# Performance work log

Measured on AMD Instinct MI355X. Metric: run time of the kernel, lower is better.

The kernel has to match this reference:

```python
import jax, jax.numpy as jnp
import numpy as np
from jax import lax


def _lstm_last(x, w_ih, w_hh, b_ih, b_hh):
    # x: [N, T, F]; PyTorch single-layer LSTM, gate order i,f,g,o. Returns last h: [N, H].
    N, T, F = x.shape
    H = w_hh.shape[1]
    x_proj = jnp.einsum('ntf,gf->tng', x, w_ih) + (b_ih + b_hh)  # [T, N, 4H]

    def step(carry, xp):
        h, c = carry
        gates = xp + h @ w_hh.T
        i, f, g, o = jnp.split(gates, 4, axis=-1)
        c = jax.nn.sigmoid(f) * c + jax.nn.sigmoid(i) * jnp.tanh(g)
        h = jax.nn.sigmoid(o) * jnp.tanh(c)
        return (h, c), None

    h0 = jnp.zeros((N, H), x.dtype)
    (h, _), _ = lax.scan(step, (h0, h0), x_proj)
    return h


def _gcn_conv(x, w, b, src, dst, n_nodes):
    # PyG GCNConv: h = D^{-1/2} (A+I) D^{-1/2} (x @ w) + b
    h = x @ w  # [N, out]
    loops = jnp.arange(n_nodes, dtype=src.dtype)
    s = jnp.concatenate([src, loops])
    d = jnp.concatenate([dst, loops])
    deg = jax.ops.segment_sum(jnp.ones_like(d, dtype=h.dtype), d, num_segments=n_nodes)
    dinv = jnp.where(deg > 0, lax.rsqrt(deg), 0.0)
    norm = dinv[s] * dinv[d]  # [E+N]
    msgs = h[s] * norm[:, None]
    out = jax.ops.segment_sum(msgs, d, num_segments=n_nodes)
    return out + b


def setup_inputs() -> dict:
    key = jax.random.key(0)
    ks = jax.random.split(key, 8)
    N, T, F, H, E, C = 50000, 32, 64, 256, 1600000, 2
    s = 0.05
    return {
        'x': jax.random.normal(ks[0], (N, T, F), jnp.float32),
        'edge_index': jax.random.randint(ks[1], (2, E), 0, N, jnp.int64),
        'w_ih': jax.random.normal(ks[2], (4 * H, F), jnp.float32) * s,
        'w_hh': jax.random.normal(ks[3], (4 * H, H), jnp.float32) * s,
        'b_ih': jnp.zeros((4 * H,), jnp.float32),
        'b_hh': jnp.zeros((4 * H,), jnp.float32),
        'w1': jax.random.normal(ks[4], (H, H), jnp.float32) * s,
        'b1': jnp.zeros((H,), jnp.float32),
        'w2': jax.random.normal(ks[5], (H, H // 2), jnp.float32) * s,
        'b2': jnp.zeros((H // 2,), jnp.float32),
        'wc': jax.random.normal(ks[6], (H // 2, C), jnp.float32) * s,
        'bc': jnp.zeros((C,), jnp.float32),
    }


def reference(x, edge_index, w_ih, w_hh, b_ih, b_hh, w1, b1, w2, b2, wc, bc):
    n_nodes = x.shape[0]
    src, dst = edge_index[0], edge_index[1]
    feats = _lstm_last(x, w_ih, w_hh, b_ih, b_hh)          # [N, H]
    feats = jax.nn.relu(_gcn_conv(feats, w1, b1, src, dst, n_nodes))
    feats = jax.nn.relu(_gcn_conv(feats, w2, b2, src, dst, n_nodes))
    logits = feats @ wc + bc
    return jax.nn.softmax(logits, axis=1)
```

## Files before the change

### kernel.cpp

```cpp
#include <hip/hip_runtime.h>
#include <cstdint>
#include <cstddef>

typedef __attribute__((ext_vector_type(8))) short s16x8;
typedef __attribute__((ext_vector_type(4))) float f32x4;
typedef __attribute__((ext_vector_type(4))) unsigned int u32x4;

#define DEV static __device__ __forceinline__

DEV unsigned short f2bf(float f){
  unsigned u = __builtin_bit_cast(unsigned, f);
  unsigned r = u + 0x7FFFu + ((u >> 16) & 1u);
  return (unsigned short)(r >> 16);
}
DEV float bf2f(unsigned short s){
  unsigned u = ((unsigned)s) << 16;
  return __builtin_bit_cast(float, u);
}
DEV float sigf(float v){ return 1.0f / (1.0f + __expf(-v)); }
DEV float tanh_f(float v){ return 1.0f - 2.0f / (__expf(2.0f*v) + 1.0f); }

#define NT 32
#define NF 64
#define NHID 256
#define MR 112
#define RT 7

__global__ void pack_lstm_kernel(const float* __restrict__ w_ih,
                                 const float* __restrict__ w_hh,
                                 unsigned short* __restrict__ wp){
  int idx = blockIdx.x*256 + threadIdx.x;
  if (idx >= 64*10*64) return;
  int lane = idx & 63;
  int kc = (idx >> 6) % 10;
  int ct = idx / 640;
  int col = ct*16 + (lane & 15);
  int kb = kc*32 + (lane >> 4)*8;
#pragma unroll
  for (int j = 0; j < 8; ++j){
    int k = kb + j;
    float v = (k < 256) ? w_hh[(size_t)col*256 + k] : w_ih[(size_t)col*64 + (k-256)];
    wp[(size_t)idx*8 + j] = f2bf(v);
  }
}

__global__ void pack_gemm_kernel(const float* __restrict__ wsrc,
                                 unsigned short* __restrict__ bp,
                                 int nout, int nct){
  int idx = blockIdx.x*256 + threadIdx.x;
  if (idx >= nct*8*64) return;
  int lane = idx & 63;
  int kc = (idx >> 6) & 7;
  int ct = idx >> 9;
  int col = ct*16 + (lane & 15);
  int kb = kc*32 + (lane >> 4)*8;
#pragma unroll
  for (int j = 0; j < 8; ++j)
    bp[(size_t)idx*8 + j] = f2bf(wsrc[(size_t)(kb + j)*nout + col]);
}

__global__ void bias_kernel(const float* __restrict__ bi, const float* __restrict__ bh,
                            float* __restrict__ bias){
  int i = blockIdx.x*256 + threadIdx.x;
  if (i < 1024) bias[i] = bi[i] + bh[i];
}

__global__ void init_nodes_kernel(int* cnt, int* fill, int nn){
  int i = blockIdx.x*256 + threadIdx.x;
  if (i < nn){ cnt[i] = 0; fill[i] = 0; }
}
__global__ void count_kernel(const int* __restrict__ dst, int* cnt, int ne){
  int e = blockIdx.x*256 + threadIdx.x;
  if (e < ne) atomicAdd(&cnt[dst[e]], 1);
}
__global__ void dinv_kernel(const int* __restrict__ cnt, float* dinv, int nn){
  int i = blockIdx.x*256 + threadIdx.x;
  if (i < nn) dinv[i] = rsqrtf((float)(cnt[i] + 1));
}
__global__ void scan_kernel(const int* __restrict__ cnt, int* __restrict__ rp, int nn){
  __shared__ int sums[1024];
  int tid = threadIdx.x;
  int chunk = (nn + 1023) >> 10;
  int beg = tid * chunk, end = beg + chunk; if (end > nn) end = nn; if (beg > nn) beg = nn;
  int s = 0;
  for (int i = beg; i < end; ++i) s += cnt[i];
  sums[tid] = s; __syncthreads();
  for (int off = 1; off < 1024; off <<= 1){
    int add = (tid >= off) ? sums[tid - off] : 0;
    __syncthreads();
    sums[tid] += add;
    __syncthreads();
  }
  int run = (tid > 0) ? sums[tid - 1] : 0;
  for (int i = beg; i < end; ++i){ rp[i] = run; run += cnt[i]; }
  if (tid == 0) rp[nn] = sums[1023];
}
__global__ void fill_kernel(const int* __restrict__ src, const int* __restrict__ dst,
                            const int* __restrict__ rp, int* fill, int* ci, int ne){
  int e = blockIdx.x*256 + threadIdx.x;
  if (e < ne){
    int d = dst[e];
    int p = atomicAdd(&fill[d], 1);
    ci[rp[d] + p] = src[e];
  }
}

DEV void load_x16p(const float* p, unsigned* xs32){
#pragma unroll
  for (int i = 0; i < 4; ++i){
    f32x4 v = ((const f32x4*)p)[i];
    xs32[i*2]   = (unsigned)f2bf(v[0]) | ((unsigned)f2bf(v[1]) << 16);
    xs32[i*2+1] = (unsigned)f2bf(v[2]) | ((unsigned)f2bf(v[3]) << 16);
  }
}

__global__ __launch_bounds__(512, 2)
void lstm_kernel(const float* __restrict__ x, const s16x8* __restrict__ wp,
                 const float* __restrict__ bias, unsigned short* __restrict__ feats0,
                 int nn){
  extern __shared__ char smem[];
  unsigned short (*h_lds)[MR][264] = (unsigned short (*)[MR][264])smem;
  unsigned short (*x_lds)[72] = (unsigned short (*)[72])(smem + (size_t)2*MR*264*2);

  const int tid = threadIdx.x;
  const int w = tid >> 6;
  const int l = tid & 63;
  const int lrow = l & 15;
  const int lhi = l >> 4;
  const int base = blockIdx.x * MR;

  float bv[2][4];
#pragma unroll
  for (int p = 0; p < 2; ++p)
#pragma unroll
    for (int g = 0; g < 4; ++g)
      bv[p][g] = bias[g*256 + (p*8 + w)*16 + lrow];

  float c[2][RT][4];
#pragma unroll
  for (int p = 0; p < 2; ++p)
#pragma unroll
    for (int r = 0; r < RT; ++r)
#pragma unroll
      for (int q = 0; q < 4; ++q) c[p][r][q] = 0.0f;

  {
    unsigned* hz = (unsigned*)smem;
    for (int i = tid; i < MR*264/2; i += 512) hz[i] = 0u;
  }

  const bool xact = (tid < 448);
  const int xr = tid >> 2, xc = tid & 3;
  long xnode = base + xr; if (xnode >= nn) xnode = nn - 1;
  const float* xb = x + (size_t)xnode * NT * NF + xc * 16;

  unsigned xs32[8];
  if (xact){
    load_x16p(xb, xs32);
    u32x4 a = {xs32[0], xs32[1], xs32[2], xs32[3]};
    u32x4 b = {xs32[4], xs32[5], xs32[6], xs32[7]};
    *(u32x4*)&x_lds[xr][xc*16]     = a;
    *(u32x4*)&x_lds[xr][xc*16 + 8] = b;
  }
  __syncthreads();

  for (int t = 0; t < NT; ++t){
    const int tb = t & 1;
    if (xact && (t + 1 < NT)) load_x16p(xb + (size_t)(t+1)*NF, xs32);

#pragma unroll
    for (int p = 0; p < 2; ++p){
      const int ut = p*8 + w;
      f32x4 acc[RT][4];
#pragma unroll
      for (int r = 0; r < RT; ++r)
#pragma unroll
        for (int g = 0; g < 4; ++g)
          acc[r][g] = (f32x4){bv[p][g], bv[p][g], bv[p][g], bv[p][g]};

#pragma unroll
      for (int kc = 0; kc < 10; ++kc){
        s16x8 bfr[4];
#pragma unroll
        for (int g = 0; g < 4; ++g){
          int ct = g*16 + ut;
          bfr[g] = wp[(size_t)(ct*10 + kc)*64 + l];
        }
#pragma unroll
        for (int r = 0; r < RT; ++r){
          s16x8 afr;
          if (kc < 8)
            afr = *(const s16x8*)&h_lds[tb][r*16 + lrow][kc*32 + lhi*8];
          else
            afr = *(const s16x8*)&x_lds[r*16 + lrow][(kc-8)*32 + lhi*8];
#pragma unroll
          for (int g = 0; g < 4; ++g)
            acc[r][g] = __builtin_amdgcn_mfma_f32_16x16x32_bf16(afr, bfr[g], acc[r][g], 0, 0, 0);
        }
      }
#pragma unroll
      for (int r = 0; r < RT; ++r){
#pragma unroll
        for (int q = 0; q < 4; ++q){
          float iv = acc[r][0][q];
          float fv = acc[r][1][q];
          float gv = acc[r][2][q];
          float ov = acc[r][3][q];
          float cv = c[p][r][q];
          cv = sigf(fv)*cv + sigf(iv)*tanh_f(gv);
          c[p][r][q] = cv;
          float hv = sigf(ov)*tanh_f(cv);
          h_lds[tb^1][r*16 + lhi*4 + q][ut*16 + lrow] = f2bf(hv);
        }
      }
    }
    __syncthreads();
    if (xact && (t + 1 < NT)){
      u32x4 a = {xs32[0], xs32[1], xs32[2], xs32[3]};
      u32x4 b = {xs32[4], xs32[5], xs32[6], xs32[7]};
      *(u32x4*)&x_lds[xr][xc*16]     = a;
      *(u32x4*)&x_lds[xr][xc*16 + 8] = b;
    }
    __syncthreads();
  }

#pragma unroll
  for (int i = 0; i < 7; ++i){
    int ch = i*512 + tid;
    int row = ch >> 5, cc = ch & 31;
    long node = base + row;
    if (node < nn){
      s16x8 v = *(const s16x8*)&h_lds[0][row][cc*8];
      *(s16x8*)&feats0[(size_t)node*256 + cc*8] = v;
    }
  }
}

template<int CTPW, int NOUT>
__global__ __launch_bounds__(256)
void gemm_kernel(const unsigned short* __restrict__ A, const s16x8* __restrict__ Bp,
                 unsigned short* __restrict__ Cout, int nn){
  __shared__ __align__(16) unsigned short a_lds[64][264];
  const int tid = threadIdx.x, w = tid >> 6, l = tid & 63, lrow = l & 15, lhi = l >> 4;
  const long m0 = (long)blockIdx.x * 64;
#pragma unroll
  for (int i = 0; i < 8; ++i){
    int ch = i*256 + tid;
    int row = ch >> 5, cc = ch & 31;
    long node = m0 + row; if (node >= nn) node = nn - 1;
    s16x8 v = *(const s16x8*)&A[(size_t)node*256 + cc*8];
    *(s16x8*)&a_lds[row][cc*8] = v;
  }
  __syncthreads();
  f32x4 acc[4][CTPW];
#pragma unroll
  for (int r = 0; r < 4; ++r)
#pragma unroll
    for (int j = 0; j < CTPW; ++j) acc[r][j] = (f32x4){0.f,0.f,0.f,0.f};
#pragma unroll
  for (int kc = 0; kc < 8; ++kc){
    s16x8 bfr[CTPW];
#pragma unroll
    for (int j = 0; j < CTPW; ++j)
      bfr[j] = Bp[(size_t)((w*CTPW + j)*8 + kc)*64 + l];
#pragma unroll
    for (int r = 0; r < 4; ++r){
      s16x8 afr = *(const s16x8*)&a_lds[r*16 + lrow][kc*32 + lhi*8];
#pragma unroll
      for (int j = 0; j < CTPW; ++j)
        acc[r][j] = __builtin_amdgcn_mfma_f32_16x16x32_bf16(afr, bfr[j], acc[r][j], 0, 0, 0);
    }
  }
#pragma unroll
  for (int r = 0; r < 4; ++r)
#pragma unroll
    for (int j = 0; j < CTPW; ++j){
      int col = (w*CTPW + j)*16 + lrow;
#pragma unroll
      for (int q = 0; q < 4; ++q){
        long node = m0 + r*16 + lhi*4 + q;
        if (node < nn) Cout[(size_t)node*NOUT + col] = f2bf(acc[r][j][q]);
      }
    }
}

template<int D>
__global__ __launch_bounds__(256)
void gather_kernel(const unsigned short* __restrict__ tmp, const int* __restrict__ rp,
                   const int* __restrict__ ci, const float* __restrict__ dinv,
                   const float* __restrict__ bvec, unsigned short* __restrict__ outf,
                   int nn){
  const int l = threadIdx.x & 63;
  const int d = blockIdx.x*4 + (threadIdx.x >> 6);
  if (d >= nn) return;
  constexpr int C = D / 64;
  float dv = dinv[d];
  float acc[C];
  if constexpr (D == 256){
    uint2 u = *((const uint2*)(tmp + (size_t)d*256) + l);
    float w0 = dv*dv;
    acc[0] = w0*bf2f((unsigned short)(u.x & 0xffff));
    acc[1] = w0*bf2f((unsigned short)(u.x >> 16));
    acc[2] = w0*bf2f((unsigned short)(u.y & 0xffff));
    acc[3] = w0*bf2f((unsigned short)(u.y >> 16));
  } else {
    unsigned u = *((const unsigned*)(tmp + (size_t)d*128) + l);
    float w0 = dv*dv;
    acc[0] = w0*bf2f((unsigned short)(u & 0xffff));
    acc[1] = w0*bf2f((unsigned short)(u >> 16));
  }
  int e0 = rp[d], e1 = rp[d+1];
  for (int e = e0; e < e1; ++e){
    int s = ci[e];
    float wgt = dv * dinv[s];
    if constexpr (D == 256){
      uint2 u = *((const uint2*)(tmp + (size_t)s*256) + l);
      acc[0] += wgt*bf2f((unsigned short)(u.x & 0xffff));
      acc[1] += wgt*bf2f((unsigned short)(u.x >> 16));
      acc[2] += wgt*bf2f((unsigned short)(u.y & 0xffff));
      acc[3] += wgt*bf2f((unsigned short)(u.y >> 16));
    } else {
      unsigned u = *((const unsigned*)(tmp + (size_t)s*128) + l);
      acc[0] += wgt*bf2f((unsigned short)(u & 0xffff));
      acc[1] += wgt*bf2f((unsigned short)(u >> 16));
    }
  }
  if constexpr (D == 256){
    float o0 = fmaxf(acc[0] + bvec[l*4+0], 0.f);
    float o1 = fmaxf(acc[1] + bvec[l*4+1], 0.f);
    float o2 = fmaxf(acc[2] + bvec[l*4+2], 0.f);
    float o3 = fmaxf(acc[3] + bvec[l*4+3], 0.f);
    uint2 o;
    o.x = (unsigned)f2bf(o0) | ((unsigned)f2bf(o1) << 16);
    o.y = (unsigned)f2bf(o2) | ((unsigned)f2bf(o3) << 16);
    *((uint2*)(outf + (size_t)d*256) + l) = o;
  } else {
    float o0 = fmaxf(acc[0] + bvec[l*2+0], 0.f);
    float o1 = fmaxf(acc[1] + bvec[l*2+1], 0.f);
    *((unsigned*)(outf + (size_t)d*128) + l) = (unsigned)f2bf(o0) | ((unsigned)f2bf(o1) << 16);
  }
}

__global__ __launch_bounds__(256)
void head_kernel(const unsigned short* __restrict__ feats2, const float* __restrict__ wc,
                 const float* __restrict__ bc, float* __restrict__ out, int nn){
  int n = blockIdx.x*256 + threadIdx.x;
  if (n >= nn) return;
  const uint2* row = (const uint2*)(feats2 + (size_t)n*128);
  float d0 = bc[0], d1 = bc[1];
#pragma unroll
  for (int b = 0; b < 32; ++b){
    uint2 u = row[b];
    float f0 = bf2f((unsigned short)(u.x & 0xffff));
    float f1 = bf2f((unsigned short)(u.x >> 16));
    float f2 = bf2f((unsigned short)(u.y & 0xffff));
    float f3 = bf2f((unsigned short)(u.y >> 16));
    int k = b*4;
    d0 += f0*wc[k*2+0] + f1*wc[(k+1)*2+0] + f2*wc[(k+2)*2+0] + f3*wc[(k+3)*2+0];
    d1 += f0*wc[k*2+1] + f1*wc[(k+1)*2+1] + f2*wc[(k+2)*2+1] + f3*wc[(k+3)*2+1];
  }
  float m = fmaxf(d0, d1);
  float e0 = __expf(d0 - m), e1 = __expf(d1 - m);
  float inv = 1.0f / (e0 + e1);
  ((float2*)out)[n] = make_float2(e0*inv, e1*inv);
}

extern "C" void kernel_launch(void* const* d_in, const int* in_sizes, int n_in,
                              void* d_out, int out_size, void* d_ws, size_t ws_size,
                              hipStream_t stream){
  const float* x     = (const float*)d_in[0];
  const int*   ei    = (const int*)d_in[1];
  const float* w_ih  = (const float*)d_in[2];
  const float* w_hh  = (const float*)d_in[3];
  const float* b_ih  = (const float*)d_in[4];
  const float* b_hh  = (const float*)d_in[5];
  const float* w1    = (const float*)d_in[6];
  const float* b1    = (const float*)d_in[7];
  const float* w2    = (const float*)d_in[8];
  const float* b2    = (const float*)d_in[9];
  const float* wc    = (const float*)d_in[10];
  const float* bc    = (const float*)d_in[11];
  float* out = (float*)d_out;

  const int nn = in_sizes[0] / (NT*NF);
  const int ne = in_sizes[1] / 2;
  const int* src = ei;
  const int* dst = ei + ne;

  char* wsp = (char*)d_ws;
  size_t off = 0;
  auto alloc = [&](size_t bytes) -> void* {
    void* p = wsp + off;
    off += (bytes + 255) & ~(size_t)255;
    return p;
  };
  unsigned short* wp     = (unsigned short*)alloc((size_t)64*10*64*8*2);
  float* bias            = (float*)alloc(1024*4);
  unsigned short* w1p    = (unsigned short*)alloc((size_t)16*8*64*8*2);
  unsigned short* w2p    = (unsigned short*)alloc((size_t)8*8*64*8*2);
  int* cnt               = (int*)alloc((size_t)nn*4);
  float* dinv            = (float*)alloc((size_t)nn*4);
  int* rp                = (int*)alloc(((size_t)nn+1)*4);
  int* fillc             = (int*)alloc((size_t)nn*4);
  int* ci                = (int*)alloc((size_t)ne*4);
  unsigned short* slotA  = (unsigned short*)alloc((size_t)nn*256*2);
  unsigned short* slotB  = (unsigned short*)alloc((size_t)nn*256*2);
  unsigned short* feats0 = slotA;
  unsigned short* tmp1   = slotB;
  unsigned short* feats1 = slotA;
  unsigned short* tmp2   = slotB;
  unsigned short* feats2 = slotB + (size_t)nn*128;
  (void)ws_size; (void)n_in; (void)out_size;

  const int nb = (nn + 255)/256;
  const int eb = (ne + 255)/256;

  hipLaunchKernelGGL(pack_lstm_kernel, dim3(160), dim3(256), 0, stream, w_ih, w_hh, wp);
  hipLaunchKernelGGL(pack_gemm_kernel, dim3(32), dim3(256), 0, stream, w1, w1p, 256, 16);
  hipLaunchKernelGGL(pack_gemm_kernel, dim3(16), dim3(256), 0, stream, w2, w2p, 128, 8);
  hipLaunchKernelGGL(bias_kernel, dim3(4), dim3(256), 0, stream, b_ih, b_hh, bias);
  hipLaunchKernelGGL(init_nodes_kernel, dim3(nb), dim3(256), 0, stream, cnt, fillc, nn);
  hipLaunchKernelGGL(count_kernel, dim3(eb), dim3(256), 0, stream, dst, cnt, ne);
  hipLaunchKernelGGL(dinv_kernel, dim3(nb), dim3(256), 0, stream, cnt, dinv, nn);
  hipLaunchKernelGGL(scan_kernel, dim3(1), dim3(1024), 0, stream, cnt, rp, nn);
  hipLaunchKernelGGL(fill_kernel, dim3(eb), dim3(256), 0, stream, src, dst, rp, fillc, ci, ne);

  const int lwg = (nn + MR - 1)/MR;
  const size_t lstm_lds = (size_t)2*MR*264*2 + (size_t)MR*72*2;
  hipLaunchKernelGGL(lstm_kernel, dim3(lwg), dim3(512), lstm_lds, stream,
                     x, (const s16x8*)wp, bias, feats0, nn);

  const int gwg = (nn + 63)/64;
  const int awg = (nn + 3)/4;
  hipLaunchKernelGGL((gemm_kernel<4,256>), dim3(gwg), dim3(256), 0, stream,
                     feats0, (const s16x8*)w1p, tmp1, nn);
  hipLaunchKernelGGL((gather_kernel<256>), dim3(awg), dim3(256), 0, stream,
                     tmp1, rp, ci, dinv, b1, feats1, nn);
  hipLaunchKernelGGL((gemm_kernel<2,128>), dim3(gwg), dim3(256), 0, stream,
                     feats1, (const s16x8*)w2p, tmp2, nn);
  hipLaunchKernelGGL((gather_kernel<128>), dim3(awg), dim3(256), 0, stream,
                     tmp2, rp, ci, dinv, b2, feats2, nn);
  hipLaunchKernelGGL(head_kernel, dim3(nb), dim3(256), 0, stream, feats2, wc, bc, out, nn);
}
```

Before: 3.934 ms.

## Restructure LSTM kernel to 1024 threads, 64 rows, double-buffered x

```diff
diff --git a/kernel.cpp b/kernel.cpp
--- a/kernel.cpp
+++ b/kernel.cpp
@@ -4,7 +4,6 @@
 
 typedef __attribute__((ext_vector_type(8))) short s16x8;
 typedef __attribute__((ext_vector_type(4))) float f32x4;
-typedef __attribute__((ext_vector_type(4))) unsigned int u32x4;
 
 #define DEV static __device__ __forceinline__
 
@@ -23,8 +22,8 @@
 #define NT 32
 #define NF 64
 #define NHID 256
-#define MR 112
-#define RT 7
+#define MR 64
+#define RT 4
 
 __global__ void pack_lstm_kernel(const float* __restrict__ w_ih,
                                  const float* __restrict__ w_hh,
@@ -105,22 +104,13 @@
   }
 }
 
-DEV void load_x16p(const float* p, unsigned* xs32){
-#pragma unroll
-  for (int i = 0; i < 4; ++i){
-    f32x4 v = ((const f32x4*)p)[i];
-    xs32[i*2]   = (unsigned)f2bf(v[0]) | ((unsigned)f2bf(v[1]) << 16);
-    xs32[i*2+1] = (unsigned)f2bf(v[2]) | ((unsigned)f2bf(v[3]) << 16);
-  }
-}
-
-__global__ __launch_bounds__(512, 2)
+__global__ __launch_bounds__(1024, 4)
 void lstm_kernel(const float* __restrict__ x, const s16x8* __restrict__ wp,
                  const float* __restrict__ bias, unsigned short* __restrict__ feats0,
                  int nn){
   extern __shared__ char smem[];
   unsigned short (*h_lds)[MR][264] = (unsigned short (*)[MR][264])smem;
-  unsigned short (*x_lds)[72] = (unsigned short (*)[72])(smem + (size_t)2*MR*264*2);
+  unsigned short (*x_lds)[MR][72] = (unsigned short (*)[MR][72])(smem + (size_t)2*MR*264*2);
 
   const int tid = threadIdx.x;
   const int w = tid >> 6;
@@ -129,104 +119,93 @@
   const int lhi = l >> 4;
   const int base = blockIdx.x * MR;
 
-  float bv[2][4];
-#pragma unroll
-  for (int p = 0; p < 2; ++p)
-#pragma unroll
-    for (int g = 0; g < 4; ++g)
-      bv[p][g] = bias[g*256 + (p*8 + w)*16 + lrow];
-
-  float c[2][RT][4];
-#pragma unroll
-  for (int p = 0; p < 2; ++p)
-#pragma unroll
-    for (int r = 0; r < RT; ++r)
-#pragma unroll
-      for (int q = 0; q < 4; ++q) c[p][r][q] = 0.0f;
+  float bv[4];
+#pragma unroll
+  for (int g = 0; g < 4; ++g)
+    bv[g] = bias[g*256 + w*16 + lrow];
+
+  float c[RT][4];
+#pragma unroll
+  for (int r = 0; r < RT; ++r)
+#pragma unroll
+    for (int q = 0; q < 4; ++q) c[r][q] = 0.0f;
 
   {
     unsigned* hz = (unsigned*)smem;
-    for (int i = tid; i < MR*264/2; i += 512) hz[i] = 0u;
-  }
-
-  const bool xact = (tid < 448);
-  const int xr = tid >> 2, xc = tid & 3;
+    for (int i = tid; i < MR*264/2; i += 1024) hz[i] = 0u;
+  }
+
+  const int xr = tid >> 4, xc = tid & 15;
   long xnode = base + xr; if (xnode >= nn) xnode = nn - 1;
-  const float* xb = x + (size_t)xnode * NT * NF + xc * 16;
-
-  unsigned xs32[8];
-  if (xact){
-    load_x16p(xb, xs32);
-    u32x4 a = {xs32[0], xs32[1], xs32[2], xs32[3]};
-    u32x4 b = {xs32[4], xs32[5], xs32[6], xs32[7]};
-    *(u32x4*)&x_lds[xr][xc*16]     = a;
-    *(u32x4*)&x_lds[xr][xc*16 + 8] = b;
+  const float* xb_ptr = x + (size_t)xnode * NT * NF + xc * 4;
+
+  {
+    f32x4 v = *(const f32x4*)xb_ptr;
+    uint2 s;
+    s.x = (unsigned)f2bf(v[0]) | ((unsigned)f2bf(v[1]) << 16);
+    s.y = (unsigned)f2bf(v[2]) | ((unsigned)f2bf(v[3]) << 16);
+    *(uint2*)&x_lds[0][xr][xc*4] = s;
   }
   __syncthreads();
 
+  int tb = 0, xbuf = 0;
   for (int t = 0; t < NT; ++t){
-    const int tb = t & 1;
-    if (xact && (t + 1 < NT)) load_x16p(xb + (size_t)(t+1)*NF, xs32);
-
-#pragma unroll
-    for (int p = 0; p < 2; ++p){
-      const int ut = p*8 + w;
-      f32x4 acc[RT][4];
-#pragma unroll
-      for (int r = 0; r < RT; ++r)
+    uint2 xs;
+    const bool pf = (t + 1 < NT);
+    if (pf){
+      f32x4 v = *(const f32x4*)(xb_ptr + (size_t)(t+1)*NF);
+      xs.x = (unsigned)f2bf(v[0]) | ((unsigned)f2bf(v[1]) << 16);
+      xs.y = (unsigned)f2bf(v[2]) | ((unsigned)f2bf(v[3]) << 16);
+    }
+
+    f32x4 acc[RT][4];
+#pragma unroll
+    for (int r = 0; r < RT; ++r)
+#pragma unroll
+      for (int g = 0; g < 4; ++g)
+        acc[r][g] = (f32x4){bv[g], bv[g], bv[g], bv[g]};
+
+#pragma unroll
+    for (int kc = 0; kc < 10; ++kc){
+      s16x8 bfr[4];
+#pragma unroll
+      for (int g = 0; g < 4; ++g)
+        bfr[g] = wp[(size_t)((g*16 + w)*10 + kc)*64 + l];
+#pragma unroll
+      for (int r = 0; r < RT; ++r){
+        s16x8 afr;
+        if (kc < 8)
+          afr = *(const s16x8*)&h_lds[tb][r*16 + lrow][kc*32 + lhi*8];
+        else
+          afr = *(const s16x8*)&x_lds[xbuf][r*16 + lrow][(kc-8)*32 + lhi*8];
 #pragma unroll
         for (int g = 0; g < 4; ++g)
-          acc[r][g] = (f32x4){bv[p][g], bv[p][g], bv[p][g], bv[p][g]};
-
-#pragma unroll
-      for (int kc = 0; kc < 10; ++kc){
-        s16x8 bfr[4];
-#pragma unroll
-        for (int g = 0; g < 4; ++g){
-          int ct = g*16 + ut;
-          bfr[g] = wp[(size_t)(ct*10 + kc)*64 + l];
-        }
-#pragma unroll
-        for (int r = 0; r < RT; ++r){
-          s16x8 afr;
-          if (kc < 8)
-            afr = *(const s16x8*)&h_lds[tb][r*16 + lrow][kc*32 + lhi*8];
-          else
-            afr = *(const s16x8*)&x_lds[r*16 + lrow][(kc-8)*32 + lhi*8];
-#pragma unroll
-          for (int g = 0; g < 4; ++g)
-            acc[r][g] = __builtin_amdgcn_mfma_f32_16x16x32_bf16(afr, bfr[g], acc[r][g], 0, 0, 0);
-        }
+          acc[r][g] = __builtin_amdgcn_mfma_f32_16x16x32_bf16(afr, bfr[g], acc[r][g], 0, 0, 0);
       }
-#pragma unroll
-      for (int r = 0; r < RT; ++r){
-#pragma unroll
-        for (int q = 0; q < 4; ++q){
-          float iv = acc[r][0][q];
-          float fv = acc[r][1][q];
-          float gv = acc[r][2][q];
-          float ov = acc[r][3][q];
-          float cv = c[p][r][q];
-          cv = sigf(fv)*cv + sigf(iv)*tanh_f(gv);
-          c[p][r][q] = cv;
-          float hv = sigf(ov)*tanh_f(cv);
-          h_lds[tb^1][r*16 + lhi*4 + q][ut*16 + lrow] = f2bf(hv);
-        }
+    }
+#pragma unroll
+    for (int r = 0; r < RT; ++r){
+#pragma unroll
+      for (int q = 0; q < 4; ++q){
+        float iv = acc[r][0][q];
+        float fv = acc[r][1][q];
+        float gv = acc[r][2][q];
+        float ov = acc[r][3][q];
+        float cv = c[r][q];
+        cv = sigf(fv)*cv + sigf(iv)*tanh_f(gv);
+        c[r][q] = cv;
+        float hv = sigf(ov)*tanh_f(cv);
+        h_lds[tb^1][r*16 + lhi*4 + q][w*16 + lrow] = f2bf(hv);
       }
     }
+    if (pf) *(uint2*)&x_lds[xbuf^1][xr][xc*4] = xs;
     __syncthreads();
-    if (xact && (t + 1 < NT)){
-      u32x4 a = {xs32[0], xs32[1], xs32[2], xs32[3]};
-      u32x4 b = {xs32[4], xs32[5], xs32[6], xs32[7]};
-      *(u32x4*)&x_lds[xr][xc*16]     = a;
-      *(u32x4*)&x_lds[xr][xc*16 + 8] = b;
-    }
-    __syncthreads();
-  }
-
-#pragma unroll
-  for (int i = 0; i < 7; ++i){
-    int ch = i*512 + tid;
+    tb ^= 1; xbuf ^= 1;
+  }
+
+#pragma unroll
+  for (int i = 0; i < 2; ++i){
+    int ch = i*1024 + tid;
     int row = ch >> 5, cc = ch & 31;
     long node = base + row;
     if (node < nn){
@@ -426,8 +405,8 @@
   hipLaunchKernelGGL(fill_kernel, dim3(eb), dim3(256), 0, stream, src, dst, rp, fillc, ci, ne);
 
   const int lwg = (nn + MR - 1)/MR;
-  const size_t lstm_lds = (size_t)2*MR*264*2 + (size_t)MR*72*2;
-  hipLaunchKernelGGL(lstm_kernel, dim3(lwg), dim3(512), lstm_lds, stream,
+  const size_t lstm_lds = (size_t)2*MR*264*2 + (size_t)2*MR*72*2;
+  hipLaunchKernelGGL(lstm_kernel, dim3(lwg), dim3(1024), lstm_lds, stream,
                      x, (const s16x8*)wp, bias, feats0, nn);
 
   const int gwg = (nn + 63)/64;
```

New measurement: 4.727 ms. 1.2x slower.
